# Optimization experiments

Measured on AMD Instinct MI355X. Metric: run time of the kernel, lower is better.

The kernel has to match this reference:

```python
import jax, jax.numpy as jnp
import numpy as np

RADIUS = 5
EPS = 1e-08


def _box_blur(x, r):
    """Normalized (2r+1)x(2r+1) box filter with reflect padding, NCHW."""
    k = 2 * r + 1
    B, C, H, W = x.shape
    xp = jnp.pad(x, ((0, 0), (0, 0), (r, r), (r, r)), mode='reflect')
    y = xp.reshape(B * C, 1, H + 2 * r, W + 2 * r)
    kh = jnp.ones((1, 1, k, 1), x.dtype) / k
    kw = jnp.ones((1, 1, 1, k), x.dtype) / k
    y = jax.lax.conv_general_dilated(y, kh, (1, 1), 'VALID')
    y = jax.lax.conv_general_dilated(y, kw, (1, 1), 'VALID')
    return y.reshape(B, C, H, W)


def setup_inputs() -> dict:
    key = jax.random.key(0)
    k1, k2 = jax.random.split(key)
    feat = jax.random.uniform(k1, (8, 16, 512, 512), dtype=jnp.float32)
    img = jax.random.uniform(k2, (8, 1, 512, 512), dtype=jnp.float32)
    return {"feat": feat, "img": img}


def reference(feat, img):
    r, eps = RADIUS, EPS
    # scalar-guidance guided filter (guidance img has 1 channel)
    mean_I = _box_blur(img, r)                  # [B,1,H,W]
    mean_p = _box_blur(feat, r)                 # [B,D,H,W]
    corr_I = _box_blur(img * img, r)            # [B,1,H,W]
    corr_Ip = _box_blur(img * feat, r)          # [B,D,H,W]
    var_I = corr_I - mean_I * mean_I
    cov_Ip = corr_Ip - mean_I * mean_p
    a = cov_Ip / (var_I + eps)                  # [B,D,H,W]
    b = mean_p - a * mean_I                     # [B,D,H,W]
    mean_a = _box_blur(a, r)
    mean_b = _box_blur(b, r)
    return mean_a * img + mean_b
```

## Files before the change

### kernel.cpp

```cpp
#include <hip/hip_runtime.h>

#define HH 512
#define WW 512
#define HW (512*512)
#define NB 8
#define ND 16
#define TW 64
#define TH 32
#define VR 42
#define PT 86

__device__ __forceinline__ int reflect(int v) {
    if (v < 0) v = -v;
    if (v >= HH) v = 2*HH - 2 - v;
    return v;
}

__global__ __launch_bounds__(256) void img_stats(const float* __restrict__ img,
                                                 float2* __restrict__ miv) {
    const int EE = 42, Q = 43, PH = 33;
    __shared__ float sI[EE*Q], sI2[EE*Q];
    __shared__ float hI[EE*PH], hI2[EE*PH];

    int blk  = blockIdx.x;
    int tile = blk & 255;
    int b    = blk >> 8;
    int ty0  = (tile >> 4) * 32;
    int tx0  = (tile & 15) * 32;
    const float* ib = img + (size_t)b*HW;
    const float inv121 = 1.0f/121.0f;

    for (int i = threadIdx.x; i < EE*EE; i += 256) {
        int y = i / EE, x = i - y*EE;
        int gy = reflect(ty0 - 5 + y);
        int gx = reflect(tx0 - 5 + x);
        float v = ib[gy*WW + gx];
        sI [y*Q + x] = v;
        sI2[y*Q + x] = v*v;
    }
    __syncthreads();
    if (threadIdx.x < 168) {
        int t = threadIdx.x;
        int arr = t / 84, r2 = t - arr*84;
        int seg = r2 / 42, row = r2 - seg*42;
        const float* sr = (arr ? sI2 : sI) + row*Q;
        float* dr = (arr ? hI2 : hI) + row*PH;
        int x0 = seg*16;
        float s = 0.f;
        #pragma unroll
        for (int j = 0; j < 10; ++j) s += sr[x0+j];
        #pragma unroll
        for (int x = 0; x < 16; ++x) {
            s += sr[x0+x+10];
            dr[x0+x] = s;
            s -= sr[x0+x];
        }
    }
    __syncthreads();
    {
        int t = threadIdx.x;
        int arr = t >> 7, r2 = t & 127;
        int seg = r2 >> 5, col = r2 & 31;
        const float* src = arr ? hI2 : hI;
        float* dst = arr ? sI2 : sI;
        int y0 = seg*8;
        float s = 0.f;
        #pragma unroll
        for (int j = 0; j < 10; ++j) s += src[(y0+j)*PH+col];
        #pragma unroll
        for (int k = 0; k < 8; ++k) {
            int y = y0 + k;
            s += src[(y+10)*PH+col];
            dst[y*Q+col] = s;
            s -= src[y*PH+col];
        }
    }
    __syncthreads();
    for (int i = threadIdx.x; i < 32*32; i += 256) {
        int y = i >> 5, x = i & 31;
        float mI  = sI [y*Q+x]*inv121;
        float mII = sI2[y*Q+x]*inv121;
        float var = mII - mI*mI;
        int gy = ty0 + y, gx = tx0 + x;
        float2 o; o.x = mI; o.y = 1.0f / (var + 1e-8f);
        miv[(size_t)b*HW + gy*WW + gx] = o;
    }
}

__global__ __launch_bounds__(256) void guided_main(const float* __restrict__ feat,
                                                   const float* __restrict__ img,
                                                   const float2* __restrict__ miv,
                                                   float* __restrict__ out) {
    __shared__ __align__(16) float hF[VR*PT];
    __shared__ __align__(16) float hP[VR*PT];

    int blk  = blockIdx.x;
    int tile = blk & 127;
    int bd   = blk >> 7;
    int b    = bd >> 4;
    int ty0  = (tile >> 3) * TH;
    int tx0  = (tile & 7)  * TW;

    const float inv121 = 1.0f/121.0f;
    const float* fb   = feat + (size_t)bd*HW;
    const float* ib   = img  + (size_t)b*HW;
    const float2* mivb = miv + (size_t)b*HW;
    const int t = threadIdx.x;

    if (t < 252) {
        int seg = t / 84, col = t - seg*84;
        int gx = reflect(tx0 - 10 + col);
        const float* fcol = fb + gx;
        const float* icol = ib + gx;
        int vr0 = seg*14;
        float rf[11], rp[11];
        float sf = 0.f, sp = 0.f;
        #pragma unroll
        for (int j = 0; j < 10; ++j) {
            int gy = reflect(ty0 - 10 + vr0 + j);
            float f = fcol[gy*WW], im = icol[gy*WW];
            float p = f*im;
            rf[j] = f; rp[j] = p; sf += f; sp += p;
        }
        #pragma unroll
        for (int k = 0; k < 14; ++k) {
            int vr = vr0 + k;
            int gy = reflect(ty0 + vr);
            float f = fcol[gy*WW], im = icol[gy*WW];
            float p = f*im;
            sf += f; sp += p;
            hF[vr*PT + col] = sf;
            hP[vr*PT + col] = sp;
            sf -= rf[k%11]; sp -= rp[k%11];
            rf[(k+10)%11] = f; rp[(k+10)%11] = p;
        }
    }
    __syncthreads();

    if (t < 168) {
        int arr = t & 1;
        int j2  = t >> 1;
        int seg = (j2 >= 42) ? 1 : 0;
        int vr  = j2 - seg*42;
        int xb = seg ? 38 : 0;
        int nout = seg ? 18 : 19;
        float* rA = (arr ? hP : hF) + vr*PT;
        float2 ring[5];
        float T = 0.f;
        #pragma unroll
        for (int j = 0; j < 5; ++j) {
            float2 v = *(float2*)(rA + xb + 2*j);
            ring[j] = v; T += v.x + v.y;
        }
        #pragma unroll
        for (int k2 = 0; k2 < 19; ++k2) {
            if (k2 < nout) {
                int hc = xb + 2*k2;
                float2 p = *(float2*)(rA + hc + 10);
                float2 q = ring[k2 % 5];
                float O0 = T + p.x;
                float O1 = O0 + p.y - q.x;
                T = O1 - q.y;
                ring[k2 % 5] = p;
                float2 o; o.x = O0*inv121; o.y = O1*inv121;
                *(float2*)(rA + hc + 10*seg) = o;
            }
        }
    }
    __syncthreads();

    for (int i = t; i < VR*37; i += 256) {
        int y = i / 37, c2 = i - y*37;
        int x0 = 2*c2;
        int slot = x0 + ((x0 >= 38) ? 10 : 0);
        float* pF = &hF[y*PT + slot];
        float* pP = &hP[y*PT + slot];
        float2 mp2  = *(float2*)pF;
        float2 cip2 = *(float2*)pP;
        int gy = reflect(ty0 - 5 + y);
        const float2* mrow = mivb + gy*WW;
        int gx0 = tx0 - 5 + x0;
        float2 g0 = mrow[reflect(gx0)];
        float2 g1 = mrow[reflect(gx0+1)];
        float a0 = (cip2.x - g0.x*mp2.x) * g0.y;
        float b0 = mp2.x - a0*g0.x;
        float a1 = (cip2.y - g1.x*mp2.y) * g1.y;
        float b1 = mp2.y - a1*g1.x;
        float2 oa; oa.x = a0; oa.y = a1;
        float2 ob2; ob2.x = b0; ob2.y = b1;
        *(float2*)pF = oa;
        *(float2*)pP = ob2;
    }
    __syncthreads();

    if (t < 148) {
        int arr = t & 1;
        int j2  = t >> 1;
        int seg = (j2 >= 37) ? 1 : 0;
        int c2  = j2 - seg*37;
        int x0 = 2*c2;
        int slotc = x0 + ((x0 >= 38) ? 10 : 0);
        int y0 = seg*16;
        float* A = (arr ? hP : hF);
        float2 ring[11];
        float sx = 0.f, sy = 0.f;
        #pragma unroll
        for (int j = 0; j < 10; ++j) {
            float2 v = *(float2*)(A + (y0+j)*PT + slotc);
            ring[j] = v; sx += v.x; sy += v.y;
        }
        #pragma unroll
        for (int k = 0; k < 16; ++k) {
            int y = y0 + k;
            float2 v = *(float2*)(A + (y+10)*PT + slotc);
            sx += v.x; sy += v.y;
            int wrow = y + 10*seg;
            float2 o; o.x = sx; o.y = sy;
            *(float2*)(A + wrow*PT + slotc) = o;
            sx -= ring[k%11].x; sy -= ring[k%11].y;
            ring[(k+10)%11] = v;
        }
    }
    __syncthreads();

    if (t < 128) {
        int arr = t & 1;
        int r2  = t >> 1;
        int seg = r2 >> 5, row = r2 & 31;
        int prow = row + ((row >= 16) ? 10 : 0);
        float* rA = (arr ? hP : hF) + prow*PT;
        int xb = seg*32;
        float2 ring[5];
        float T = 0.f;
        #pragma unroll
        for (int j = 0; j < 5; ++j) {
            int idx = xb + 2*j;
            int sl = idx + ((idx >= 38) ? 10 : 0);
            float2 v = *(float2*)(rA + sl);
            ring[j] = v; T += v.x + v.y;
        }
        #pragma unroll
        for (int k2 = 0; k2 < 16; ++k2) {
            int x = xb + 2*k2;
            int idx = x + 10;
            int sl = idx + ((idx >= 38) ? 10 : 0);
            float2 p = *(float2*)(rA + sl);
            float2 q = ring[k2 % 5];
            float O0 = T + p.x;
            float O1 = O0 + p.y - q.x;
            T = O1 - q.y;
            ring[k2 % 5] = p;
            int wcol = x + 20*seg;
            float2 o; o.x = O0; o.y = O1;
            *(float2*)(rA + wcol) = o;
        }
    }
    __syncthreads();

    float* ob = out + (size_t)bd*HW;
    for (int i = t; i < TH*32; i += 256) {
        int y = i >> 5, c2 = i & 31;
        int x0 = 2*c2;
        int prow = y + ((y >= 16) ? 10 : 0);
        int wcol = (x0 < 32) ? x0 : x0 + 20;
        float2 ma2 = *(float2*)(&hF[prow*PT + wcol]);
        float2 mb2 = *(float2*)(&hP[prow*PT + wcol]);
        int gy = ty0 + y;
        float2 im2 = *(const float2*)(ib + gy*WW + tx0 + x0);
        float2 o;
        o.x = (ma2.x*im2.x + mb2.x)*inv121;
        o.y = (ma2.y*im2.y + mb2.y)*inv121;
        *(float2*)(ob + gy*WW + tx0 + x0) = o;
    }
}

extern "C" void kernel_launch(void* const* d_in, const int* in_sizes, int n_in,
                              void* d_out, int out_size, void* d_ws, size_t ws_size,
                              hipStream_t stream) {
    const float* feat = (const float*)d_in[0];
    const float* img  = (const float*)d_in[1];
    float* out  = (float*)d_out;
    float2* miv = (float2*)d_ws;

    img_stats<<<NB*256, 256, 0, stream>>>(img, miv);
    guided_main<<<NB*ND*128, 256, 0, stream>>>(feat, img, miv, out);
}
```

Baseline: 153.3 us.

## Fuse a/b coefficient compute into horizontal pass and final output into last pass

The first horizontal box-sum pass now has one thread handle both the mean_p and corr_Ip rows and compute the a/b coefficients inline, which removes a separate elementwise phase and its barrier. The final horizontal pass likewise computes both mean_a and mean_b per thread and writes the output directly, removing the last shared-memory round trip and a barrier. The trade-off is fewer active threads per phase (84 and 128 instead of 168 and 128 with half the work each), longer serial chains per thread and more register use.

```diff
diff --git a/kernel.cpp b/kernel.cpp
--- a/kernel.cpp
+++ b/kernel.cpp
@@ -137,59 +137,55 @@
     }
     __syncthreads();
 
-    if (t < 168) {
-        int arr = t & 1;
-        int j2  = t >> 1;
-        int seg = (j2 >= 42) ? 1 : 0;
-        int vr  = j2 - seg*42;
-        int xb = seg ? 38 : 0;
+    if (t < 84) {
+        int seg = (t >= 42) ? 1 : 0;
+        int vr  = t - seg*42;
+        int xb  = seg ? 38 : 0;
         int nout = seg ? 18 : 19;
-        float* rA = (arr ? hP : hF) + vr*PT;
-        float2 ring[5];
-        float T = 0.f;
+        float* rF = hF + vr*PT;
+        float* rP = hP + vr*PT;
+        int gy = reflect(ty0 - 5 + vr);
+        const float2* mrow = mivb + gy*WW;
+        float2 ringF[5], ringP[5];
+        float TF = 0.f, TP = 0.f;
         #pragma unroll
         for (int j = 0; j < 5; ++j) {
-            float2 v = *(float2*)(rA + xb + 2*j);
-            ring[j] = v; T += v.x + v.y;
+            float2 vF = *(float2*)(rF + xb + 2*j);
+            float2 vP = *(float2*)(rP + xb + 2*j);
+            ringF[j] = vF; TF += vF.x + vF.y;
+            ringP[j] = vP; TP += vP.x + vP.y;
         }
         #pragma unroll
         for (int k2 = 0; k2 < 19; ++k2) {
             if (k2 < nout) {
                 int hc = xb + 2*k2;
-                float2 p = *(float2*)(rA + hc + 10);
-                float2 q = ring[k2 % 5];
-                float O0 = T + p.x;
-                float O1 = O0 + p.y - q.x;
-                T = O1 - q.y;
-                ring[k2 % 5] = p;
-                float2 o; o.x = O0*inv121; o.y = O1*inv121;
-                *(float2*)(rA + hc + 10*seg) = o;
+                float2 pF = *(float2*)(rF + hc + 10);
+                float2 pP = *(float2*)(rP + hc + 10);
+                float2 qF = ringF[k2 % 5];
+                float2 qP = ringP[k2 % 5];
+                float O0f = TF + pF.x;
+                float O1f = O0f + pF.y - qF.x;
+                TF = O1f - qF.y;
+                ringF[k2 % 5] = pF;
+                float O0p = TP + pP.x;
+                float O1p = O0p + pP.y - qP.x;
+                TP = O1p - qP.y;
+                ringP[k2 % 5] = pP;
+                float mp0  = O0f*inv121, mp1  = O1f*inv121;
+                float cip0 = O0p*inv121, cip1 = O1p*inv121;
+                int gx0 = tx0 - 5 + hc;
+                float2 g0 = mrow[reflect(gx0)];
+                float2 g1 = mrow[reflect(gx0+1)];
+                float a0 = (cip0 - g0.x*mp0) * g0.y;
+                float b0 = mp0 - a0*g0.x;
+                float a1 = (cip1 - g1.x*mp1) * g1.y;
+                float b1 = mp1 - a1*g1.x;
+                float2 oa; oa.x = a0; oa.y = a1;
+                float2 ob2; ob2.x = b0; ob2.y = b1;
+                *(float2*)(rF + hc + 10*seg) = oa;
+                *(float2*)(rP + hc + 10*seg) = ob2;
             }
         }
-    }
-    __syncthreads();
-
-    for (int i = t; i < VR*37; i += 256) {
-        int y = i / 37, c2 = i - y*37;
-        int x0 = 2*c2;
-        int slot = x0 + ((x0 >= 38) ? 10 : 0);
-        float* pF = &hF[y*PT + slot];
-        float* pP = &hP[y*PT + slot];
-        float2 mp2  = *(float2*)pF;
-        float2 cip2 = *(float2*)pP;
-        int gy = reflect(ty0 - 5 + y);
-        const float2* mrow = mivb + gy*WW;
-        int gx0 = tx0 - 5 + x0;
-        float2 g0 = mrow[reflect(gx0)];
-        float2 g1 = mrow[reflect(gx0+1)];
-        float a0 = (cip2.x - g0.x*mp2.x) * g0.y;
-        float b0 = mp2.x - a0*g0.x;
-        float a1 = (cip2.y - g1.x*mp2.y) * g1.y;
-        float b1 = mp2.y - a1*g1.x;
-        float2 oa; oa.x = a0; oa.y = a1;
-        float2 ob2; ob2.x = b0; ob2.y = b1;
-        *(float2*)pF = oa;
-        *(float2*)pP = ob2;
     }
     __syncthreads();
 
@@ -223,54 +219,52 @@
     }
     __syncthreads();
 
-    if (t < 128) {
-        int arr = t & 1;
-        int r2  = t >> 1;
-        int seg = r2 >> 5, row = r2 & 31;
-        int prow = row + ((row >= 16) ? 10 : 0);
-        float* rA = (arr ? hP : hF) + prow*PT;
-        int xb = seg*32;
-        float2 ring[5];
-        float T = 0.f;
-        #pragma unroll
-        for (int j = 0; j < 5; ++j) {
-            int idx = xb + 2*j;
-            int sl = idx + ((idx >= 38) ? 10 : 0);
-            float2 v = *(float2*)(rA + sl);
-            ring[j] = v; T += v.x + v.y;
-        }
-        #pragma unroll
-        for (int k2 = 0; k2 < 16; ++k2) {
-            int x = xb + 2*k2;
-            int idx = x + 10;
-            int sl = idx + ((idx >= 38) ? 10 : 0);
-            float2 p = *(float2*)(rA + sl);
-            float2 q = ring[k2 % 5];
-            float O0 = T + p.x;
-            float O1 = O0 + p.y - q.x;
-            T = O1 - q.y;
-            ring[k2 % 5] = p;
-            int wcol = x + 20*seg;
-            float2 o; o.x = O0; o.y = O1;
-            *(float2*)(rA + wcol) = o;
-        }
-    }
-    __syncthreads();
-
-    float* ob = out + (size_t)bd*HW;
-    for (int i = t; i < TH*32; i += 256) {
-        int y = i >> 5, c2 = i & 31;
-        int x0 = 2*c2;
-        int prow = y + ((y >= 16) ? 10 : 0);
-        int wcol = (x0 < 32) ? x0 : x0 + 20;
-        float2 ma2 = *(float2*)(&hF[prow*PT + wcol]);
-        float2 mb2 = *(float2*)(&hP[prow*PT + wcol]);
-        int gy = ty0 + y;
-        float2 im2 = *(const float2*)(ib + gy*WW + tx0 + x0);
-        float2 o;
-        o.x = (ma2.x*im2.x + mb2.x)*inv121;
-        o.y = (ma2.y*im2.y + mb2.y)*inv121;
-        *(float2*)(ob + gy*WW + tx0 + x0) = o;
+    {
+        float* ob = out + (size_t)bd*HW;
+        if (t < 128) {
+            int row = t & 31, seg = t >> 5;
+            int prow = row + ((row >= 16) ? 10 : 0);
+            const float* rA = hF + prow*PT;
+            const float* rB = hP + prow*PT;
+            int xb = seg*16;
+            float2 ringA[5], ringB[5];
+            float TA = 0.f, TB = 0.f;
+            #pragma unroll
+            for (int j = 0; j < 5; ++j) {
+                int idx = xb + 2*j;
+                int sl = idx + ((idx >= 38) ? 10 : 0);
+                float2 vA = *(float2*)(rA + sl);
+                float2 vB = *(float2*)(rB + sl);
+                ringA[j] = vA; TA += vA.x + vA.y;
+                ringB[j] = vB; TB += vB.x + vB.y;
+            }
+            int gy = ty0 + row;
+            const float* irow = ib + gy*WW + tx0;
+            float* orow = ob + gy*WW + tx0;
+            #pragma unroll
+            for (int k2 = 0; k2 < 8; ++k2) {
+                int x = xb + 2*k2;
+                int idx = x + 10;
+                int sl = idx + ((idx >= 38) ? 10 : 0);
+                float2 pA = *(float2*)(rA + sl);
+                float2 pB = *(float2*)(rB + sl);
+                float2 qA = ringA[k2 % 5];
+                float2 qB = ringB[k2 % 5];
+                float A0 = TA + pA.x;
+                float A1 = A0 + pA.y - qA.x;
+                TA = A1 - qA.y;
+                ringA[k2 % 5] = pA;
+                float B0 = TB + pB.x;
+                float B1 = B0 + pB.y - qB.x;
+                TB = B1 - qB.y;
+                ringB[k2 % 5] = pB;
+                float2 im2 = *(const float2*)(irow + x);
+                float2 o;
+                o.x = (A0*im2.x + B0)*inv121;
+                o.y = (A1*im2.y + B1)*inv121;
+                *(float2*)(orow + x) = o;
+            }
+        }
     }
 }
 
```

New measurement: 203.2 us. +32.5%, slower.

## Restructure img_stats to reuse guided_main tiling with register-ring vertical sums

Applied to the files above, without the earlier changes.

The image statistics kernel now uses the same 32x64 tile and shared-memory layout as the main kernel. Vertical box sums are computed straight from global memory with register ring buffers, and horizontal sums use float2 sliding windows written back in place. Halving the block count reduces redundant halo loads and sync phases in this prologue kernel. It is a small part of total time, since the main kernel dominates, and it adds indexing complexity in the in-place horizontal pass.

```diff
diff --git a/kernel.cpp b/kernel.cpp
--- a/kernel.cpp
+++ b/kernel.cpp
@@ -18,72 +18,88 @@
 
 __global__ __launch_bounds__(256) void img_stats(const float* __restrict__ img,
                                                  float2* __restrict__ miv) {
-    const int EE = 42, Q = 43, PH = 33;
-    __shared__ float sI[EE*Q], sI2[EE*Q];
-    __shared__ float hI[EE*PH], hI2[EE*PH];
+    __shared__ __align__(16) float hF[VR*PT];
+    __shared__ __align__(16) float hP[VR*PT];
 
     int blk  = blockIdx.x;
-    int tile = blk & 255;
-    int b    = blk >> 8;
-    int ty0  = (tile >> 4) * 32;
-    int tx0  = (tile & 15) * 32;
+    int tile = blk & 127;
+    int b    = blk >> 7;
+    int ty0  = (tile >> 3) * TH;
+    int tx0  = (tile & 7)  * TW;
+
+    const float inv121 = 1.0f/121.0f;
     const float* ib = img + (size_t)b*HW;
-    const float inv121 = 1.0f/121.0f;
-
-    for (int i = threadIdx.x; i < EE*EE; i += 256) {
-        int y = i / EE, x = i - y*EE;
-        int gy = reflect(ty0 - 5 + y);
-        int gx = reflect(tx0 - 5 + x);
-        float v = ib[gy*WW + gx];
-        sI [y*Q + x] = v;
-        sI2[y*Q + x] = v*v;
-    }
-    __syncthreads();
-    if (threadIdx.x < 168) {
-        int t = threadIdx.x;
-        int arr = t / 84, r2 = t - arr*84;
-        int seg = r2 / 42, row = r2 - seg*42;
-        const float* sr = (arr ? sI2 : sI) + row*Q;
-        float* dr = (arr ? hI2 : hI) + row*PH;
-        int x0 = seg*16;
-        float s = 0.f;
-        #pragma unroll
-        for (int j = 0; j < 10; ++j) s += sr[x0+j];
-        #pragma unroll
-        for (int x = 0; x < 16; ++x) {
-            s += sr[x0+x+10];
-            dr[x0+x] = s;
-            s -= sr[x0+x];
-        }
-    }
-    __syncthreads();
-    {
-        int t = threadIdx.x;
-        int arr = t >> 7, r2 = t & 127;
-        int seg = r2 >> 5, col = r2 & 31;
-        const float* src = arr ? hI2 : hI;
-        float* dst = arr ? sI2 : sI;
-        int y0 = seg*8;
-        float s = 0.f;
-        #pragma unroll
-        for (int j = 0; j < 10; ++j) s += src[(y0+j)*PH+col];
-        #pragma unroll
-        for (int k = 0; k < 8; ++k) {
-            int y = y0 + k;
-            s += src[(y+10)*PH+col];
-            dst[y*Q+col] = s;
-            s -= src[y*PH+col];
-        }
-    }
-    __syncthreads();
-    for (int i = threadIdx.x; i < 32*32; i += 256) {
-        int y = i >> 5, x = i & 31;
-        float mI  = sI [y*Q+x]*inv121;
-        float mII = sI2[y*Q+x]*inv121;
+    const int t = threadIdx.x;
+
+    if (t < 252) {
+        int seg = t / 84, col = t - seg*84;
+        int gx = reflect(tx0 - 10 + col);
+        const float* icol = ib + gx;
+        int vr0 = seg*14;
+        float rv[11], rq[11];
+        float sv = 0.f, sq = 0.f;
+        #pragma unroll
+        for (int j = 0; j < 10; ++j) {
+            int gy = reflect(ty0 - 10 + vr0 + j);
+            float v = icol[gy*WW], q = v*v;
+            rv[j] = v; rq[j] = q; sv += v; sq += q;
+        }
+        #pragma unroll
+        for (int k = 0; k < 14; ++k) {
+            int vr = vr0 + k;
+            int gy = reflect(ty0 + vr);
+            float v = icol[gy*WW], q = v*v;
+            sv += v; sq += q;
+            hF[vr*PT + col] = sv;
+            hP[vr*PT + col] = sq;
+            sv -= rv[k%11]; sq -= rq[k%11];
+            rv[(k+10)%11] = v; rq[(k+10)%11] = q;
+        }
+    }
+    __syncthreads();
+
+    if (t < 168) {
+        int arr = t & 1;
+        int j2  = t >> 1;
+        int seg = (j2 >= 42) ? 1 : 0;
+        int vr  = j2 - seg*42;
+        int xb = seg ? 38 : 0;
+        int nout = seg ? 18 : 19;
+        float* rA = (arr ? hP : hF) + vr*PT;
+        float2 ring[5];
+        float T = 0.f;
+        #pragma unroll
+        for (int j = 0; j < 5; ++j) {
+            float2 v = *(float2*)(rA + xb + 2*j);
+            ring[j] = v; T += v.x + v.y;
+        }
+        #pragma unroll
+        for (int k2 = 0; k2 < 19; ++k2) {
+            if (k2 < nout) {
+                int hc = xb + 2*k2;
+                float2 p = *(float2*)(rA + hc + 10);
+                float2 q = ring[k2 % 5];
+                float O0 = T + p.x;
+                float O1 = O0 + p.y - q.x;
+                T = O1 - q.y;
+                ring[k2 % 5] = p;
+                float2 o; o.x = O0*inv121; o.y = O1*inv121;
+                *(float2*)(rA + hc + 10*seg) = o;
+            }
+        }
+    }
+    __syncthreads();
+
+    float2* mb = miv + (size_t)b*HW;
+    for (int i = t; i < TH*TW; i += 256) {
+        int y = i >> 6, x = i & 63;
+        int vr = y + 5, hc = x + 5;
+        int slot = hc + ((hc >= 38) ? 10 : 0);
+        float mI  = hF[vr*PT + slot];
+        float mII = hP[vr*PT + slot];
         float var = mII - mI*mI;
-        int gy = ty0 + y, gx = tx0 + x;
         float2 o; o.x = mI; o.y = 1.0f / (var + 1e-8f);
-        miv[(size_t)b*HW + gy*WW + gx] = o;
+        mb[(ty0 + y)*WW + tx0 + x] = o;
     }
 }
 
@@ -282,6 +298,6 @@
     float* out  = (float*)d_out;
     float2* miv = (float2*)d_ws;
 
-    img_stats<<<NB*256, 256, 0, stream>>>(img, miv);
+    img_stats<<<NB*128, 256, 0, stream>>>(img, miv);
     guided_main<<<NB*ND*128, 256, 0, stream>>>(feat, img, miv, out);
 }
```

Result: no change. 150.7 us (-1.7%).
